# Kernel tuning notes

Measured on AMD Instinct MI355X. Metric: run time of the kernel, lower is better.

## Reference

```python
import jax, jax.numpy as jnp
import numpy as np

D = 2048
NH = 16
DH = D // NH          # 128
DC = D // 4           # 512  (KV latent)
DCQ = D // 2          # 1024 (Q latent)
B = 1
L = 2048
MAX_LEN = 4096


def precompute_rope(dh, max_len):
    inv_freq = 1.0 / (10000.0 ** (jnp.arange(0, dh, 2, dtype=jnp.float32) / dh))
    t = jnp.arange(max_len, dtype=jnp.float32)
    freqs = jnp.outer(t, inv_freq)                 # [max_len, dh/2]
    emb = jnp.concatenate([freqs, freqs], axis=-1) # [max_len, dh]
    return jnp.cos(emb), jnp.sin(emb)


def apply_rope(t, cos, sin):
    # t: [B, H, L, dh]; cos/sin: [L, dh]
    x1, x2 = jnp.split(t, 2, axis=-1)
    rot = jnp.concatenate([-x2, x1], axis=-1)
    return t * cos + rot * sin


def setup_inputs() -> dict:
    key = jax.random.key(0)
    ks = jax.random.split(key, 9)
    s = 0.02
    return {
        "x": jax.random.normal(ks[0], (B, L, D), dtype=jnp.float32),
        "W_DKV": jax.random.normal(ks[1], (D, DC), dtype=jnp.float32) * s,
        "W_UK": jax.random.normal(ks[2], (DC, NH * DH), dtype=jnp.float32) * s,
        "W_UV": jax.random.normal(ks[3], (DC, NH * DH), dtype=jnp.float32) * s,
        "W_DQ": jax.random.normal(ks[4], (D, DCQ), dtype=jnp.float32) * s,
        "W_UQ": jax.random.normal(ks[5], (DCQ, 2 * NH * DH), dtype=jnp.float32) * s,
        "W_lam": jax.random.normal(ks[6], (D, NH), dtype=jnp.float32) * s,
        "b_lam": jnp.zeros((NH,), dtype=jnp.float32),
        "W_out": jax.random.normal(ks[7], (D, D), dtype=jnp.float32) * s,
    }


def reference(x, W_DKV, W_UK, W_UV, W_DQ, W_UQ, W_lam, b_lam, W_out):
    Bx, Lx, Dx = x.shape
    cos, sin = precompute_rope(DH, MAX_LEN)
    cos, sin = cos[:Lx], sin[:Lx]

    # MLA KV compression: single K/V shared by the paired query heads
    c_kv = x @ W_DKV                                            # [B, L, dc]
    k = (c_kv @ W_UK).reshape(Bx, Lx, NH, DH).transpose(0, 2, 1, 3)   # [B, nh, L, dh]
    v = (c_kv @ W_UV).reshape(Bx, Lx, NH, DH).transpose(0, 2, 1, 3)   # [B, nh, L, dh]

    # Low-rank Q, doubled heads for differential attention
    c_q = x @ W_DQ                                              # [B, L, dcq]
    q = (c_q @ W_UQ).reshape(Bx, Lx, 2 * NH, DH).transpose(0, 2, 1, 3)  # [B, 2nh, L, dh]

    q = apply_rope(q, cos, sin)
    k = apply_rope(k, cos, sin)

    # Group paired heads (2i, 2i+1) share k/v head i -> avoid repeat_interleave
    qp = q.reshape(Bx, NH, 2, Lx, DH)                           # [B, nh, 2, L, dh]
    scale = 1.0 / jnp.sqrt(jnp.asarray(DH, dtype=x.dtype))
    scores = jnp.einsum('bhpqd,bhkd->bhpqk', qp, k) * scale     # [B, nh, 2, L, L]
    causal = jnp.tril(jnp.ones((Lx, Lx), dtype=bool))
    scores = jnp.where(causal, scores, jnp.asarray(-jnp.inf, dtype=scores.dtype))
    probs = jax.nn.softmax(scores, axis=-1)
    attn = jnp.einsum('bhpqk,bhkd->bhpqd', probs, v)            # [B, nh, 2, L, dh]
    attn1, attn2 = attn[:, :, 0], attn[:, :, 1]                 # [B, nh, L, dh]

    # Token-specific sigmoid lambda per head
    lam = jax.nn.sigmoid(x @ W_lam + b_lam)                     # [B, L, nh]
    lam = lam.transpose(0, 2, 1)[..., None]                     # [B, nh, L, 1]

    out = (attn1 - lam * attn2).transpose(0, 2, 1, 3).reshape(Bx, Lx, Dx)
    return out @ W_out
```

## Files before the change

### kernel.cpp

```cpp
#include <hip/hip_runtime.h>
#include <cstdint>
#include <cstddef>

typedef __bf16 bf16x8 __attribute__((ext_vector_type(8)));
typedef __bf16 bf16x4 __attribute__((ext_vector_type(4)));
typedef float f32x4 __attribute__((ext_vector_type(4)));


template <int BM, bool BF16OUT>
__device__ __forceinline__ void gemm_body(const __bf16* __restrict__ A,
                                          const __bf16* __restrict__ Bt,
                                          void* __restrict__ Cv,
                                          int N, int K, int bm, int bn,
                                          __bf16* As, __bf16* Bs) {
  const int tid = threadIdx.x;
  const int w = tid >> 6;
  const int lane = tid & 63;
  const int quad = lane >> 4;
  const int l16 = lane & 15;
  constexpr int WM = (BM == 128) ? 64 : 32;
  constexpr int MI = WM / 16;
  const int wm = (w & 1) * WM;
  const int wn = (w >> 1) * 64;
  const int srow = lane >> 2;
  const int sseg = (lane & 3) * 8;

  f32x4 acc[MI][4];
#pragma unroll
  for (int i = 0; i < MI; ++i)
#pragma unroll
    for (int j = 0; j < 4; ++j) acc[i][j] = (f32x4){0.f, 0.f, 0.f, 0.f};

  for (int k0 = 0; k0 < K; k0 += 32) {
    __syncthreads();
#pragma unroll
    for (int g = 0; g < BM / 64; ++g) {
      const int grp = w + g * 4;
      const __bf16* ga = A + (size_t)(bm + grp * 16 + srow) * K + k0 + sseg;
      __builtin_amdgcn_global_load_lds(
          (const __attribute__((address_space(1))) void*)ga,
          (__attribute__((address_space(3))) void*)&As[grp * 512], 16, 0, 0);
    }
#pragma unroll
    for (int g = 0; g < 2; ++g) {
      const int grp = w + g * 4;
      const __bf16* gb = Bt + (size_t)(bn + grp * 16 + srow) * K + k0 + sseg;
      __builtin_amdgcn_global_load_lds(
          (const __attribute__((address_space(1))) void*)gb,
          (__attribute__((address_space(3))) void*)&Bs[grp * 512], 16, 0, 0);
    }
    __syncthreads();
    bf16x8 af[MI], bfr[4];
#pragma unroll
    for (int i = 0; i < MI; ++i)
      af[i] = *(const bf16x8*)&As[(wm + i * 16 + l16) * 32 + quad * 8];
#pragma unroll
    for (int j = 0; j < 4; ++j)
      bfr[j] = *(const bf16x8*)&Bs[(wn + j * 16 + l16) * 32 + quad * 8];
#pragma unroll
    for (int i = 0; i < MI; ++i)
#pragma unroll
      for (int j = 0; j < 4; ++j)
        acc[i][j] = __builtin_amdgcn_mfma_f32_16x16x32_bf16(af[i], bfr[j],
                                                            acc[i][j], 0, 0, 0);
  }
#pragma unroll
  for (int i = 0; i < MI; ++i)
#pragma unroll
    for (int j = 0; j < 4; ++j)
#pragma unroll
      for (int r = 0; r < 4; ++r) {
        const int row = bm + wm + i * 16 + quad * 4 + r;
        const int col = bn + wn + j * 16 + l16;
        if constexpr (BF16OUT)
          ((__bf16*)Cv)[(size_t)row * N + col] = (__bf16)acc[i][j][r];
        else
          ((float*)Cv)[(size_t)row * N + col] = acc[i][j][r];
      }
}

template <int BM, bool BF16OUT>
__global__ __launch_bounds__(256) void gemm_mfma(const __bf16* __restrict__ A,
                                                 const __bf16* __restrict__ Bt,
                                                 void* __restrict__ Cv,
                                                 int M, int N, int K) {
  __shared__ __bf16 As[BM * 32];
  __shared__ __bf16 Bs[128 * 32];
  gemm_body<BM, BF16OUT>(A, Bt, Cv, N, K, blockIdx.y * BM, blockIdx.x * 128, As, Bs);
}

template <int BM>
__global__ __launch_bounds__(256) void gemm_fused3(
    const __bf16* A0, const __bf16* B0, __bf16* C0, int N0, int K0, int nx0,
    const __bf16* A1, const __bf16* B1, __bf16* C1, int N1, int K1, int nx1,
    const __bf16* A2, const __bf16* B2, __bf16* C2, int N2, int K2) {
  __shared__ __bf16 As[BM * 32];
  __shared__ __bf16 Bs[128 * 32];
  const int bx = blockIdx.x;
  const __bf16 *A, *Bt;
  __bf16* C;
  int N, K, bxl;
  if (bx < nx0)            { A = A0; Bt = B0; C = C0; N = N0; K = K0; bxl = bx; }
  else if (bx < nx0 + nx1) { A = A1; Bt = B1; C = C1; N = N1; K = K1; bxl = bx - nx0; }
  else                     { A = A2; Bt = B2; C = C2; N = N2; K = K2; bxl = bx - nx0 - nx1; }
  gemm_body<BM, true>(A, Bt, (void*)C, N, K, blockIdx.y * BM, bxl * 128, As, Bs);
}

__global__ __launch_bounds__(256) void prep_all(
    const float* __restrict__ W_DKV, const float* __restrict__ W_DQ,
    const float* __restrict__ W_UK,  const float* __restrict__ W_UV,
    const float* __restrict__ W_UQ,  const float* __restrict__ W_out,
    const float* __restrict__ x,     const float* __restrict__ W_lam,
    __bf16* __restrict__ tDKV, __bf16* __restrict__ tDQ,
    __bf16* __restrict__ tUK,  __bf16* __restrict__ tUV,
    __bf16* __restrict__ tUQ,  __bf16* __restrict__ tOut,
    __bf16* __restrict__ x_bf, __bf16* __restrict__ WlT,
    float* __restrict__ cosT, float* __restrict__ sinT) {
  __shared__ float T[32][36];
  int t = blockIdx.x;
  const int tid = threadIdx.x;
  if (t < 13312) {
    const float* src; __bf16* dst; int K, N, kx, ny;
    if (t < 1024)      {            src = W_DKV; dst = tDKV; K = 2048; N = 512;  kx = t & 63; ny = t >> 6; }
    else if (t < 3072) { t -= 1024; src = W_DQ;  dst = tDQ;  K = 2048; N = 1024; kx = t & 63; ny = t >> 6; }
    else if (t < 4096) { t -= 3072; src = W_UK;  dst = tUK;  K = 512;  N = 2048; kx = t & 15; ny = t >> 4; }
    else if (t < 5120) { t -= 4096; src = W_UV;  dst = tUV;  K = 512;  N = 2048; kx = t & 15; ny = t >> 4; }
    else if (t < 9216) { t -= 5120; src = W_UQ;  dst = tUQ;  K = 1024; N = 4096; kx = t & 31; ny = t >> 5; }
    else               { t -= 9216; src = W_out; dst = tOut; K = 2048; N = 2048; kx = t & 63; ny = t >> 6; }
    const int k0 = kx * 32;
    const int n0 = ny * 32;
    const int r = tid >> 3;
    const int c = (tid & 7) * 4;
    *(float4*)&T[r][c] = *(const float4*)&src[(size_t)(k0 + r) * N + n0 + c];
    __syncthreads();
    bf16x4 o = {(__bf16)T[c + 0][r], (__bf16)T[c + 1][r],
                (__bf16)T[c + 2][r], (__bf16)T[c + 3][r]};
    *(bf16x4*)&dst[(size_t)(n0 + r) * K + k0 + c] = o;
    return;
  }
  t -= 13312;
  if (t < 4096) {
    const int i = t * 256 + tid;
    float4 v = *(const float4*)&x[(size_t)i * 4];
    bf16x4 o = {(__bf16)v.x, (__bf16)v.y, (__bf16)v.z, (__bf16)v.w};
    *(bf16x4*)&x_bf[(size_t)i * 4] = o;
    return;
  }
  t -= 4096;
  if (t < 1024) {
    const int l = t * 2 + (tid >> 7);
    const int d = tid & 127;
    const int j = d & 63;
    const float inv = exp2f(-(float)j * 0.2076205059304601f);
    const float ang = (float)l * inv;
    cosT[l * 128 + d] = cosf(ang);
    sinT[l * 128 + d] = sinf(ang);
    return;
  }
  t -= 1024;
  {
    const int i = t * 256 + tid;
    const int k = i >> 4, n = i & 15;
    WlT[(size_t)n * 2048 + k] = (__bf16)W_lam[i];
  }
}

__global__ __launch_bounds__(256) void ropek_transv(__bf16* __restrict__ k_bf,
                                                    const float* __restrict__ cosT,
                                                    const float* __restrict__ sinT,
                                                    const __bf16* __restrict__ v_bf,
                                                    __bf16* __restrict__ v_t) {
  __shared__ float row[2048];
  __shared__ __align__(16) __bf16 Ts[32][40];
  int t = blockIdx.x;
  const int tid = threadIdx.x;
  if (t < 2048) {
    __bf16* rp = k_bf + (size_t)t * 2048;
#pragma unroll
    for (int i = 0; i < 2; ++i) {
      const int e4 = (tid + 256 * i) * 4;
      bf16x4 v = *(const bf16x4*)&rp[e4];
#pragma unroll
      for (int k = 0; k < 4; ++k) row[e4 + k] = (float)v[k];
    }
    __syncthreads();
#pragma unroll
    for (int i = 0; i < 8; ++i) {
      const int e = tid + 256 * i;
      const int d = e & 127;
      const float c = cosT[t * 128 + d];
      const float s = sinT[t * 128 + d];
      const float tv = row[e];
      const int base = e & ~127;
      const float rot = (d < 64) ? -row[base + d + 64] : row[base + d - 64];
      rp[e] = (__bf16)(tv * c + rot * s);
    }
    return;
  }
  t -= 2048;
  const int l0 = (t & 63) * 32;
  const int d0 = (t >> 6) * 32;
  const int r = tid >> 3;
  const int c = (tid & 7) * 4;
  *(bf16x4*)&Ts[r][c] = *(const bf16x4*)&v_bf[(size_t)(l0 + r) * 2048 + d0 + c];
  __syncthreads();
  bf16x4 o = {Ts[c + 0][r], Ts[c + 1][r], Ts[c + 2][r], Ts[c + 3][r]};
  *(bf16x4*)&v_t[(size_t)(d0 + r) * 2048 + l0 + c] = o;
}

__global__ __launch_bounds__(256) void lam_mfma_kernel(const __bf16* __restrict__ x_bf,
                                                       const __bf16* __restrict__ WlT,
                                                       const float* __restrict__ b_lam,
                                                       float* __restrict__ lam) {
  const int tid = threadIdx.x;
  const int w = tid >> 6, lane = tid & 63, quad = lane >> 4, l16 = lane & 15;
  const int m0 = (blockIdx.x * 4 + w) * 16;
  const __bf16* xrow = x_bf + (size_t)(m0 + l16) * 2048 + quad * 8;
  const __bf16* wrow = WlT + (size_t)l16 * 2048 + quad * 8;
  f32x4 acc[4];
#pragma unroll
  for (int u = 0; u < 4; ++u) acc[u] = (f32x4){0.f, 0.f, 0.f, 0.f};
  for (int k0 = 0; k0 < 2048; k0 += 128) {
#pragma unroll
    for (int u = 0; u < 4; ++u) {
      bf16x8 a = *(const bf16x8*)&xrow[k0 + u * 32];
      bf16x8 b = *(const bf16x8*)&wrow[k0 + u * 32];
      acc[u] = __builtin_amdgcn_mfma_f32_16x16x32_bf16(a, b, acc[u], 0, 0, 0);
    }
  }
  const float bl = b_lam[l16];
#pragma unroll
  for (int r = 0; r < 4; ++r) {
    const float v = acc[0][r] + acc[1][r] + acc[2][r] + acc[3][r] + bl;
    lam[(size_t)(m0 + quad * 4 + r) * 16 + l16] = 1.0f / (1.0f + __expf(-v));
  }
}

__global__ __launch_bounds__(256, 2) void attn_kernel3(
    const __bf16* __restrict__ Qb, const __bf16* __restrict__ Kb,
    const __bf16* __restrict__ Vt, const float* __restrict__ cosT,
    const float* __restrict__ sinT, const float* __restrict__ lam,
    __bf16* __restrict__ y) {
  __shared__ __align__(16) char smem[81920];
  float (*Ex)[132] = (float(*)[132])smem;

  const int bx = blockIdx.x;
  const int hv = bx >> 8;
  const int ii = bx & 255;
  const int qt = hv ? (ii >> 4) : 31 - (ii >> 4);
  const int hk = ii & 15;
  const int q0 = qt * 64;
  const int tid = threadIdx.x;
  const int w = tid >> 6, lane = tid & 63, quad = lane >> 4, l16 = lane & 15;
  const int wrow = (w & 1) * 32;
  const int qoff = (2 * hk + (w >> 1)) * 128;
  const int kvoff = hk * 128;
  const float qscale = 0.08838834764831845f;
  char* Pw = smem + 65536 + w * (32 * 128);

  bf16x8 aq[2][4];
#pragma unroll
  for (int s = 0; s < 2; ++s) {
    const int l = q0 + wrow + s * 16 + l16;
    const size_t qbase = (size_t)l * 4096 + qoff + quad * 8;
    bf16x8 raw[4];
#pragma unroll
    for (int ks = 0; ks < 4; ++ks)
      raw[ks] = *(const bf16x8*)&Qb[qbase + ks * 32];
#pragma unroll
    for (int ks = 0; ks < 4; ++ks) {
      const float* cp = &cosT[l * 128 + ks * 32 + quad * 8];
      const float* sp = &sinT[l * 128 + ks * 32 + quad * 8];
#pragma unroll
      for (int j = 0; j < 8; ++j) {
        const float cv = cp[j];
        const float sv = sp[j];
        const float rot = (ks < 2) ? -(float)raw[ks + 2][j] : (float)raw[ks - 2][j];
        aq[s][ks][j] = (__bf16)(((float)raw[ks][j] * cv + rot * sv) * qscale);
      }
    }
  }

  auto stage = [&](int kt_, char* buf) {
    const int k0_ = kt_ * 64;
    __bf16* Ksb = (__bf16*)buf;
    __bf16* Vsb = (__bf16*)(buf + 16384);
#pragma unroll
    for (int d = 0; d < 4; ++d) {
      const int r0 = w * 16 + d * 4;
      const int row = r0 + (lane >> 4);
      const int ck = (lane & 15) ^ (row & 15);
      const __bf16* ga = Kb + (size_t)(k0_ + row) * 2048 + kvoff + ck * 8;
      __builtin_amdgcn_global_load_lds(
          (const __attribute__((address_space(1))) void*)ga,
          (__attribute__((address_space(3))) void*)&Ksb[r0 * 128], 16, 0, 0);
      const int r0v = w * 32 + d * 8;
      const int rowv = r0v + (lane >> 3);
      const int cv = (lane & 7) ^ (rowv & 7);
      const __bf16* gv = Vt + (size_t)(kvoff + rowv) * 2048 + k0_ + cv * 8;
      __builtin_amdgcn_global_load_lds(
          (const __attribute__((address_space(1))) void*)gv,
          (__attribute__((address_space(3))) void*)&Vsb[r0v * 64], 16, 0, 0);
    }
  };

  f32x4 o[2][8];
#pragma unroll
  for (int s = 0; s < 2; ++s)
#pragma unroll
    for (int i = 0; i < 8; ++i) o[s][i] = (f32x4){0.f, 0.f, 0.f, 0.f};
  float m[2] = {-1e30f, -1e30f}, lsum[2] = {0.f, 0.f};

  asm volatile("s_waitcnt vmcnt(0)" ::: "memory");
  stage(0, smem);

  for (int kt = 0; kt <= qt; ++kt) {
    const int cur = kt & 1;
    __bf16* Ks = (__bf16*)(smem + cur * 32768);
    __bf16* Vs = (__bf16*)(smem + cur * 32768 + 16384);
    const int k0 = kt * 64;
    if (kt < qt) {
      stage(kt + 1, smem + (cur ^ 1) * 32768);
      asm volatile("s_waitcnt vmcnt(8)" ::: "memory");
    } else {
      asm volatile("s_waitcnt vmcnt(0)" ::: "memory");
    }
    __builtin_amdgcn_s_barrier();
    asm volatile("" ::: "memory");
    f32x4 st[2][4];
#pragma unroll
    for (int s = 0; s < 2; ++s)
#pragma unroll
      for (int t = 0; t < 4; ++t) st[s][t] = (f32x4){0.f, 0.f, 0.f, 0.f};
    __builtin_amdgcn_s_setprio(1);
#pragma unroll
    for (int ks = 0; ks < 4; ++ks) {
#pragma unroll
      for (int t = 0; t < 4; ++t) {
        bf16x8 ak = *(bf16x8*)&Ks[(t * 16 + l16) * 128 + (((ks * 4 + quad) ^ l16) << 3)];
        st[0][t] = __builtin_amdgcn_mfma_f32_16x16x32_bf16(ak, aq[0][ks], st[0][t], 0, 0, 0);
        st[1][t] = __builtin_amdgcn_mfma_f32_16x16x32_bf16(ak, aq[1][ks], st[1][t], 0, 0, 0);
      }
    }
    __builtin_amdgcn_s_setprio(0);
    const bool masked = (kt == qt);
#pragma unroll
    for (int s = 0; s < 2; ++s) {
      const int q = q0 + wrow + s * 16 + l16;
      float rm = -1e30f;
      if (!masked) {
#pragma unroll
        for (int t = 0; t < 4; ++t)
#pragma unroll
          for (int r = 0; r < 4; ++r) rm = fmaxf(rm, st[s][t][r]);
      } else {
#pragma unroll
        for (int t = 0; t < 4; ++t)
#pragma unroll
          for (int r = 0; r < 4; ++r) {
            const int key = k0 + t * 16 + quad * 4 + r;
            if (key > q) st[s][t][r] = -1e30f;
            rm = fmaxf(rm, st[s][t][r]);
          }
      }
      rm = fmaxf(rm, __shfl_xor(rm, 16, 64));
      rm = fmaxf(rm, __shfl_xor(rm, 32, 64));
      const float mn = fmaxf(m[s], rm);
      const float alpha = __expf(m[s] - mn);
      float rs = 0.f;
#pragma unroll
      for (int t = 0; t < 4; ++t)
#pragma unroll
        for (int r = 0; r < 4; ++r) {
          st[s][t][r] = __expf(st[s][t][r] - mn);
          rs += st[s][t][r];
        }
      rs += __shfl_xor(rs, 16, 64);
      rs += __shfl_xor(rs, 32, 64);
      m[s] = mn;
      lsum[s] = lsum[s] * alpha + rs;
      const int prow = s * 16 + l16;
#pragma unroll
      for (int t = 0; t < 4; ++t) {
        bf16x4 pk = {(__bf16)st[s][t][0], (__bf16)st[s][t][1],
                     (__bf16)st[s][t][2], (__bf16)st[s][t][3]};
        const int wch = (t * 2 + (quad >> 1)) ^ (prow & 7);
        *(bf16x4*)(Pw + prow * 128 + wch * 16 + (quad & 1) * 8) = pk;
      }
#pragma unroll
      for (int r = 0; r < 4; ++r) {
        const float ar = __shfl(alpha, quad * 4 + r, 64);
#pragma unroll
        for (int nt = 0; nt < 8; ++nt) o[s][nt][r] *= ar;
      }
    }
    __builtin_amdgcn_s_setprio(1);
#pragma unroll
    for (int ks = 0; ks < 2; ++ks) {
      const int rch = ((ks * 4 + quad) ^ (l16 & 7)) << 4;
      bf16x8 pa0 = *(bf16x8*)(Pw + l16 * 128 + rch);
      bf16x8 pa1 = *(bf16x8*)(Pw + (16 + l16) * 128 + rch);
#pragma unroll
      for (int nt = 0; nt < 8; ++nt) {
        bf16x8 bv = *(bf16x8*)&Vs[(nt * 16 + l16) * 64 + (((ks * 4 + quad) ^ (l16 & 7)) << 3)];
        o[0][nt] = __builtin_amdgcn_mfma_f32_16x16x32_bf16(pa0, bv, o[0][nt], 0, 0, 0);
        o[1][nt] = __builtin_amdgcn_mfma_f32_16x16x32_bf16(pa1, bv, o[1][nt], 0, 0, 0);
      }
    }
    __builtin_amdgcn_s_setprio(0);
    asm volatile("s_waitcnt lgkmcnt(0)" ::: "memory");
    __builtin_amdgcn_s_barrier();
    asm volatile("" ::: "memory");
  }
  if (w >= 2) {
#pragma unroll
    for (int s = 0; s < 2; ++s) {
      const float linv = 1.0f / lsum[s];
#pragma unroll
      for (int r = 0; r < 4; ++r) {
        const float inv = __shfl(linv, quad * 4 + r, 64);
        const int rr = wrow + s * 16 + quad * 4 + r;
#pragma unroll
        for (int nt = 0; nt < 8; ++nt)
          Ex[rr][nt * 16 + l16] = o[s][nt][r] * inv;
      }
    }
  }
  __syncthreads();
  if (w < 2) {
#pragma unroll
    for (int s = 0; s < 2; ++s) {
      const float linv = 1.0f / lsum[s];
#pragma unroll
      for (int r = 0; r < 4; ++r) {
        const float inv = __shfl(linv, quad * 4 + r, 64);
        const int rr = wrow + s * 16 + quad * 4 + r;
        const int l = q0 + rr;
        const float lm = lam[l * 16 + hk];
        __bf16* dst = y + (size_t)l * 2048 + hk * 128;
#pragma unroll
        for (int nt = 0; nt < 8; ++nt) {
          const float v1 = o[s][nt][r] * inv;
          dst[nt * 16 + l16] = (__bf16)(v1 - lm * Ex[rr][nt * 16 + l16]);
        }
      }
    }
  }
}

extern "C" void kernel_launch(void* const* d_in, const int* in_sizes, int n_in,
                              void* d_out, int out_size, void* d_ws, size_t ws_size,
                              hipStream_t stream) {
  const float* x     = (const float*)d_in[0];
  const float* W_DKV = (const float*)d_in[1];
  const float* W_UK  = (const float*)d_in[2];
  const float* W_UV  = (const float*)d_in[3];
  const float* W_DQ  = (const float*)d_in[4];
  const float* W_UQ  = (const float*)d_in[5];
  const float* W_lam = (const float*)d_in[6];
  const float* b_lam = (const float*)d_in[7];
  const float* W_out = (const float*)d_in[8];
  float* out = (float*)d_out;

  char* ws = (char*)d_ws;
  #define MB(n) ((size_t)(n) << 20)
  __bf16* x_bf   = (__bf16*)(ws + MB(0));
  __bf16* Wt_DKV = (__bf16*)(ws + MB(8));
  __bf16* Wt_DQ  = (__bf16*)(ws + MB(10));
  __bf16* c_kv   = (__bf16*)(ws + MB(14));
  __bf16* c_q    = (__bf16*)(ws + MB(16));
  __bf16* Wt_UK  = (__bf16*)(ws + MB(20));
  __bf16* Wt_UV  = (__bf16*)(ws + MB(22));
  __bf16* Wt_UQ  = (__bf16*)(ws + MB(24));
  __bf16* k_bf   = (__bf16*)(ws + MB(32));
  __bf16* v_bf   = (__bf16*)(ws + MB(40));
  __bf16* y_bf   = (__bf16*)(ws + MB(40));
  __bf16* q_bf   = (__bf16*)(ws + MB(48));
  __bf16* v_t    = (__bf16*)(ws + MB(64));
  float*  lam    = (float*)(ws + MB(88));
  float*  cosT   = (float*)(ws + MB(89));
  float*  sinT   = (float*)(ws + MB(90));
  __bf16* WlT    = (__bf16*)(ws + MB(91));
  __bf16* Wt_out = (__bf16*)(ws + MB(92));

  prep_all<<<18560, 256, 0, stream>>>(W_DKV, W_DQ, W_UK, W_UV, W_UQ, W_out,
                                      x, W_lam,
                                      Wt_DKV, Wt_DQ, Wt_UK, Wt_UV, Wt_UQ, Wt_out,
                                      x_bf, WlT, cosT, sinT);
  gemm_fused3<64><<<dim3(12, 32), 256, 0, stream>>>(
      x_bf, Wt_DKV, c_kv, 512, 2048, 4,
      x_bf, Wt_DQ,  c_q, 1024, 2048, 8,
      x_bf, Wt_DQ,  c_q, 1024, 2048);
  lam_mfma_kernel<<<32, 256, 0, stream>>>(x_bf, WlT, b_lam, lam);
  gemm_fused3<128><<<dim3(64, 16), 256, 0, stream>>>(
      c_kv, Wt_UK, k_bf, 2048, 512, 16,
      c_kv, Wt_UV, v_bf, 2048, 512, 16,
      c_q,  Wt_UQ, q_bf, 4096, 1024);
  ropek_transv<<<6144, 256, 0, stream>>>(k_bf, cosT, sinT, v_bf, v_t);
  attn_kernel3<<<512, 256, 0, stream>>>(q_bf, k_bf, v_t, cosT, sinT, lam, y_bf);
  gemm_mfma<64, false><<<dim3(16, 32), 256, 0, stream>>>(y_bf, Wt_out, out, 2048, 2048, 2048);
}
```

Before: 332.9 us.

## Double-buffer LDS tiles in MFMA GEMM to overlap global loads with compute

The GEMM body now keeps two LDS buffers for the A and B tiles and issues the global-to-LDS loads for the next K-slice before computing the current one. Explicit vmcnt waits and raw s_barrier calls replace the two __syncthreads per iteration. The goal is to hide global load latency behind the MFMA work. The cost is double the LDS per block, which may lower occupancy, and the hand-counted vmcnt values must stay correct.

```diff
diff --git a/kernel.cpp b/kernel.cpp
--- a/kernel.cpp
+++ b/kernel.cpp
@@ -25,21 +25,15 @@
   const int srow = lane >> 2;
   const int sseg = (lane & 3) * 8;
 
-  f32x4 acc[MI][4];
-#pragma unroll
-  for (int i = 0; i < MI; ++i)
-#pragma unroll
-    for (int j = 0; j < 4; ++j) acc[i][j] = (f32x4){0.f, 0.f, 0.f, 0.f};
-
-  for (int k0 = 0; k0 < K; k0 += 32) {
-    __syncthreads();
+  auto stage = [&](int k0, int buf) {
 #pragma unroll
     for (int g = 0; g < BM / 64; ++g) {
       const int grp = w + g * 4;
       const __bf16* ga = A + (size_t)(bm + grp * 16 + srow) * K + k0 + sseg;
       __builtin_amdgcn_global_load_lds(
           (const __attribute__((address_space(1))) void*)ga,
-          (__attribute__((address_space(3))) void*)&As[grp * 512], 16, 0, 0);
+          (__attribute__((address_space(3))) void*)&As[buf * (BM * 32) + grp * 512],
+          16, 0, 0);
     }
 #pragma unroll
     for (int g = 0; g < 2; ++g) {
@@ -47,22 +41,52 @@
       const __bf16* gb = Bt + (size_t)(bn + grp * 16 + srow) * K + k0 + sseg;
       __builtin_amdgcn_global_load_lds(
           (const __attribute__((address_space(1))) void*)gb,
-          (__attribute__((address_space(3))) void*)&Bs[grp * 512], 16, 0, 0);
-    }
-    __syncthreads();
+          (__attribute__((address_space(3))) void*)&Bs[buf * 4096 + grp * 512],
+          16, 0, 0);
+    }
+  };
+
+  f32x4 acc[MI][4];
+#pragma unroll
+  for (int i = 0; i < MI; ++i)
+#pragma unroll
+    for (int j = 0; j < 4; ++j) acc[i][j] = (f32x4){0.f, 0.f, 0.f, 0.f};
+
+  asm volatile("s_waitcnt vmcnt(0)" ::: "memory");
+  stage(0, 0);
+
+  const int NIT = K >> 5;
+  for (int it = 0; it < NIT; ++it) {
+    const int cur = it & 1;
+    if (it + 1 < NIT) {
+      stage((it + 1) << 5, cur ^ 1);
+      if constexpr (BM == 64)
+        asm volatile("s_waitcnt vmcnt(3)" ::: "memory");
+      else
+        asm volatile("s_waitcnt vmcnt(4)" ::: "memory");
+    } else {
+      asm volatile("s_waitcnt vmcnt(0)" ::: "memory");
+    }
+    __builtin_amdgcn_s_barrier();
+    asm volatile("" ::: "memory");
+    const __bf16* Ab = &As[cur * (BM * 32)];
+    const __bf16* Bb = &Bs[cur * 4096];
     bf16x8 af[MI], bfr[4];
 #pragma unroll
     for (int i = 0; i < MI; ++i)
-      af[i] = *(const bf16x8*)&As[(wm + i * 16 + l16) * 32 + quad * 8];
+      af[i] = *(const bf16x8*)&Ab[(wm + i * 16 + l16) * 32 + quad * 8];
 #pragma unroll
     for (int j = 0; j < 4; ++j)
-      bfr[j] = *(const bf16x8*)&Bs[(wn + j * 16 + l16) * 32 + quad * 8];
+      bfr[j] = *(const bf16x8*)&Bb[(wn + j * 16 + l16) * 32 + quad * 8];
 #pragma unroll
     for (int i = 0; i < MI; ++i)
 #pragma unroll
       for (int j = 0; j < 4; ++j)
         acc[i][j] = __builtin_amdgcn_mfma_f32_16x16x32_bf16(af[i], bfr[j],
                                                             acc[i][j], 0, 0, 0);
+    asm volatile("s_waitcnt lgkmcnt(0)" ::: "memory");
+    __builtin_amdgcn_s_barrier();
+    asm volatile("" ::: "memory");
   }
 #pragma unroll
   for (int i = 0; i < MI; ++i)
@@ -84,8 +108,8 @@
                                                  const __bf16* __restrict__ Bt,
                                                  void* __restrict__ Cv,
                                                  int M, int N, int K) {
-  __shared__ __bf16 As[BM * 32];
-  __shared__ __bf16 Bs[128 * 32];
+  __shared__ __bf16 As[2 * BM * 32];
+  __shared__ __bf16 Bs[2 * 128 * 32];
   gemm_body<BM, BF16OUT>(A, Bt, Cv, N, K, blockIdx.y * BM, blockIdx.x * 128, As, Bs);
 }
 
@@ -94,8 +118,8 @@
     const __bf16* A0, const __bf16* B0, __bf16* C0, int N0, int K0, int nx0,
     const __bf16* A1, const __bf16* B1, __bf16* C1, int N1, int K1, int nx1,
     const __bf16* A2, const __bf16* B2, __bf16* C2, int N2, int K2) {
-  __shared__ __bf16 As[BM * 32];
-  __shared__ __bf16 Bs[128 * 32];
+  __shared__ __bf16 As[2 * BM * 32];
+  __shared__ __bf16 Bs[2 * 128 * 32];
   const int bx = blockIdx.x;
   const __bf16 *A, *Bt;
   __bf16* C;
```

Result: faster. 324.0 us (-2.7%).
